# Kernel optimization log

Measured on AMD Instinct MI355X. Metric: run time of the kernel, lower is better.

## Reference

```python
import jax, jax.numpy as jnp
import numpy as np

N_NODES = 100000
N_EDGES = 3200000
F_IN, F_HID, F_OUT = 512, 128, 32


def setup_inputs() -> dict:
    key = jax.random.key(0)
    ks = jax.random.split(key, 8)
    x = jax.random.normal(ks[0], (N_NODES, F_IN), dtype=jnp.float32)
    edge_row = jax.random.randint(ks[1], (N_EDGES,), 0, N_NODES, dtype=jnp.int32)
    edge_col = jax.random.randint(ks[2], (N_EDGES,), 0, N_NODES, dtype=jnp.int32)
    edge_val = jax.random.uniform(ks[3], (N_EDGES,), dtype=jnp.float32)
    W1 = jax.random.normal(ks[4], (F_IN, F_HID), dtype=jnp.float32) / np.sqrt(F_IN)
    b1 = jnp.zeros((F_HID,), dtype=jnp.float32)
    W2 = jax.random.normal(ks[5], (F_HID, F_OUT), dtype=jnp.float32) / np.sqrt(F_HID)
    b2 = jnp.zeros((F_OUT,), dtype=jnp.float32)
    return {"x": x, "edge_row": edge_row, "edge_col": edge_col,
            "edge_val": edge_val, "W1": W1, "b1": b1, "W2": W2, "b2": b2}


def _spmm(edge_row, edge_col, edge_val, dense):
    # out[r] = sum_{e: row[e]==r} val[e] * dense[col[e]]  (COO SpMM)
    gathered = dense[edge_col] * edge_val[:, None]  # [E, F]
    return jax.ops.segment_sum(gathered, edge_row, num_segments=N_NODES)


def reference(x, edge_row, edge_col, edge_val, W1, b1, W2, b2):
    # GraphConvolution 1: support = x@W1; out = A @ support + b1
    h = _spmm(edge_row, edge_col, edge_val, x @ W1) + b1
    h = jax.nn.relu(h)
    # GraphConvolution 2
    logits = _spmm(edge_row, edge_col, edge_val, h @ W2) + b2
    return jax.nn.log_softmax(logits, axis=1)
```

## Files before the change

kernel.cpp:

```cpp
#include <hip/hip_runtime.h>


#define NN 100000
#define NE 3200000
#define FIN 512
#define FHID 128
#define FOUT 32
#define BROWS 64
#define NBUCK 1563
#define NPART 512
#define CHUNK 6250
#define TOT (NBUCK * NPART)
#define NSCAN1 782
#define EBCAP 2560

typedef __attribute__((ext_vector_type(8))) short bf16x8;
typedef __attribute__((ext_vector_type(4))) float f32x4;

static __device__ __forceinline__ unsigned short f2bf(float f) {
    unsigned u = __float_as_uint(f);
    unsigned r = (u + 0x7FFFu + ((u >> 16) & 1u)) >> 16;
    return (unsigned short)r;
}
static __device__ __forceinline__ float bf2f(unsigned short u) {
    return __uint_as_float(((unsigned)u) << 16);
}
static __device__ __forceinline__ float bflo(unsigned u) {
    return __uint_as_float(u << 16);
}
static __device__ __forceinline__ float bfhi(unsigned u) {
    return __uint_as_float(u & 0xffff0000u);
}
static __device__ __forceinline__ bf16x8 pack8(float4 u, float4 v) {
    bf16x8 r;
    r[0] = (short)f2bf(u.x); r[1] = (short)f2bf(u.y);
    r[2] = (short)f2bf(u.z); r[3] = (short)f2bf(u.w);
    r[4] = (short)f2bf(v.x); r[5] = (short)f2bf(v.y);
    r[6] = (short)f2bf(v.z); r[7] = (short)f2bf(v.w);
    return r;
}

__global__ __launch_bounds__(256) void fused_prep_hist(const float* __restrict__ W1,
                                                       unsigned short* __restrict__ W1t,
                                                       const int* __restrict__ erow,
                                                       int* __restrict__ cntG) {
    if (blockIdx.x < NPART) {
        __shared__ int c[NBUCK];
        const int t = threadIdx.x;
        const int w = blockIdx.x;
        for (int i = t; i < NBUCK; i += 256) c[i] = 0;
        __syncthreads();
        const int e0 = w * CHUNK;
        const int e1 = min(e0 + CHUNK, NE);
        for (int e = e0 + t; e < e1; e += 256) atomicAdd(&c[erow[e] >> 6], 1);
        __syncthreads();
        for (int i = t; i < NBUCK; i += 256) cntG[w * NBUCK + i] = c[i];
    } else {
        int t = (blockIdx.x - NPART) * 256 + threadIdx.x;
        int j = t & 7;
        int c = t >> 3;
        int l = c & 63;
        int ks = (c >> 6) & 15;
        int nt = c >> 10;
        int n = nt * 16 + (l & 15);
        int k = ks * 32 + ((l >> 4) << 3) + j;
        W1t[(size_t)c * 8 + j] = f2bf(W1[k * FHID + n]);
    }
}

__global__ __launch_bounds__(256) void scan1_kernel(const int* __restrict__ cntG,
                                                    int* __restrict__ off,
                                                    int* __restrict__ partials) {
    __shared__ int s[256];
    int t = threadIdx.x;
    int i0 = blockIdx.x * 1024 + t * 4;
    int v[4];
#pragma unroll
    for (int j = 0; j < 4; ++j) {
        int i = i0 + j;
        v[j] = (i < TOT) ? cntG[(i & (NPART - 1)) * NBUCK + (i >> 9)] : 0;
    }
    int lsum = v[0] + v[1] + v[2] + v[3];
    s[t] = lsum;
    __syncthreads();
    for (int o = 1; o < 256; o <<= 1) {
        int xv = (t >= o) ? s[t - o] : 0;
        __syncthreads();
        s[t] += xv;
        __syncthreads();
    }
    if (t == 255) partials[blockIdx.x] = s[255];
    int run = s[t] - lsum;
#pragma unroll
    for (int j = 0; j < 4; ++j) {
        if (i0 + j < TOT) off[i0 + j] = run;
        run += v[j];
    }
}

__global__ __launch_bounds__(1024) void scan2_kernel(int* partials) {
    __shared__ int s[1024];
    int t = threadIdx.x;
    int v = (t < NSCAN1) ? partials[t] : 0;
    s[t] = v;
    __syncthreads();
    for (int o = 1; o < 1024; o <<= 1) {
        int xv = (t >= o) ? s[t - o] : 0;
        __syncthreads();
        s[t] += xv;
        __syncthreads();
    }
    if (t < NSCAN1) partials[t] = s[t] - v;
}

__global__ __launch_bounds__(256) void scan3_kernel(int* __restrict__ off,
                                                    const int* __restrict__ partials) {
    int add = partials[blockIdx.x];
    int i0 = blockIdx.x * 1024 + threadIdx.x * 4;
#pragma unroll
    for (int j = 0; j < 4; ++j)
        if (i0 + j < TOT) off[i0 + j] += add;
}

__global__ __launch_bounds__(256) void scatter_part(const int* __restrict__ erow,
                                                    const int* __restrict__ ecol,
                                                    const float* __restrict__ eval,
                                                    const int* __restrict__ off,
                                                    int2* __restrict__ bcolval) {
    __shared__ int pos[NBUCK];
    const int t = threadIdx.x;
    const int w = blockIdx.x;
    for (int b = t; b < NBUCK; b += 256) pos[b] = off[b * NPART + w];
    __syncthreads();
    const int e0 = w * CHUNK;
    const int e1 = min(e0 + CHUNK, NE);
    for (int e = e0 + t; e < e1; e += 256) {
        int r = erow[e];
        int idx = atomicAdd(&pos[r >> 6], 1);
        bcolval[idx] = make_int2(ecol[e] | ((r & 63) << 20), __float_as_int(eval[e]));
    }
}

__global__ __launch_bounds__(256) void bucket_to_csr(const int* __restrict__ off,
                                                     const int2* __restrict__ bcolval,
                                                     int* __restrict__ rowptr,
                                                     int2* __restrict__ epack) {
    __shared__ int cnt[BROWS];
    __shared__ int pos[BROWS];
    __shared__ int s[BROWS];
    __shared__ int2 eb[EBCAP];
    const int b = blockIdx.x;
    const int t = threadIdx.x;
    const int s0 = off[b * NPART];
    const int send = (b == NBUCK - 1) ? NE : off[(b + 1) * NPART];
    const int n = send - s0;
    const bool fits = (n <= EBCAP);
    if (t < BROWS) cnt[t] = 0;
    __syncthreads();
    int2 myv[10];
    if (fits) {
#pragma unroll
        for (int ii = 0; ii < 10; ++ii) {
            int i = t + ii * 256;
            int2 v = make_int2(0, 0);
            if (i < n) {
                v = bcolval[s0 + i];
                atomicAdd(&cnt[((unsigned)v.x) >> 20], 1);
            }
            myv[ii] = v;
        }
    } else {
        for (int i = t; i < n; i += 256)
            atomicAdd(&cnt[((unsigned)bcolval[s0 + i].x) >> 20], 1);
    }
    __syncthreads();
    int myc = (t < BROWS) ? cnt[t] : 0;
    if (t < BROWS) s[t] = myc;
    __syncthreads();
    for (int o = 1; o < BROWS; o <<= 1) {
        int xv = (t >= o && t < BROWS) ? s[t - o] : 0;
        __syncthreads();
        if (t < BROWS) s[t] += xv;
        __syncthreads();
    }
    if (t < BROWS) {
        int excl = s[t] - myc;
        pos[t] = excl;
        int row = b * BROWS + t;
        if (row < NN) rowptr[row] = s0 + excl;
    }
    if (b == 0 && t == 0) rowptr[NN] = NE;
    __syncthreads();
    if (fits) {
#pragma unroll
        for (int ii = 0; ii < 10; ++ii) {
            int i = t + ii * 256;
            if (i < n) {
                int2 v = myv[ii];
                int p = atomicAdd(&pos[((unsigned)v.x) >> 20], 1);
                eb[p] = make_int2(v.x & 0xFFFFF, v.y);
            }
        }
        __syncthreads();
        for (int i = t; i < n; i += 256) epack[s0 + i] = eb[i];
    } else {
        for (int i = t; i < n; i += 256) {
            int2 v = bcolval[s0 + i];
            int p = atomicAdd(&pos[((unsigned)v.x) >> 20], 1);
            epack[s0 + p] = make_int2(v.x & 0xFFFFF, v.y);
        }
    }
}

__global__ __launch_bounds__(256) void gemm1_mfma(const float* __restrict__ x,
                                                  const unsigned short* __restrict__ W1t,
                                                  unsigned short* __restrict__ out) {
    const int tid = threadIdx.x;
    const int lane = tid & 63;
    const int w = tid >> 6;
    const int quad = lane >> 4;
    const int m = lane & 15;
    const int row0 = blockIdx.x * 128 + w * 32;

    int rA = row0 + m;
    int rB = row0 + 16 + m;
    rA = rA < NN ? rA : NN - 1;
    rB = rB < NN ? rB : NN - 1;
    const float* pA = x + (size_t)rA * FIN + quad * 8;
    const float* pB = x + (size_t)rB * FIN + quad * 8;

    f32x4 acc[2][8];
#pragma unroll
    for (int i = 0; i < 2; ++i)
#pragma unroll
        for (int nt = 0; nt < 8; ++nt) acc[i][nt] = (f32x4){0.f, 0.f, 0.f, 0.f};

    float4 a0 = *(const float4*)pA;
    float4 a1 = *(const float4*)(pA + 4);
    float4 b0 = *(const float4*)pB;
    float4 b1 = *(const float4*)(pB + 4);

    for (int ks = 0; ks < 16; ++ks) {
        const int kn = (ks + 1) & 15;
        float4 na0 = *(const float4*)(pA + kn * 32);
        float4 na1 = *(const float4*)(pA + kn * 32 + 4);
        float4 nb0 = *(const float4*)(pB + kn * 32);
        float4 nb1 = *(const float4*)(pB + kn * 32 + 4);

        bf16x8 fA = pack8(a0, a1);
        bf16x8 fB = pack8(b0, b1);
        bf16x8 bb[8];
#pragma unroll
        for (int nt = 0; nt < 8; ++nt)
            bb[nt] = *(const bf16x8*)(W1t + ((size_t)((nt * 16 + ks) * 64 + lane)) * 8);
#pragma unroll
        for (int nt = 0; nt < 8; ++nt) {
            acc[0][nt] = __builtin_amdgcn_mfma_f32_16x16x32_bf16(fA, bb[nt], acc[0][nt], 0, 0, 0);
            acc[1][nt] = __builtin_amdgcn_mfma_f32_16x16x32_bf16(fB, bb[nt], acc[1][nt], 0, 0, 0);
        }
        a0 = na0; a1 = na1; b0 = nb0; b1 = nb1;
    }

    const int crow0 = blockIdx.x * 128 + w * 32;
#pragma unroll
    for (int i = 0; i < 2; ++i)
#pragma unroll
        for (int nt = 0; nt < 8; ++nt) {
            int col = nt * 16 + m;
#pragma unroll
            for (int r = 0; r < 4; ++r) {
                int row = crow0 + i * 16 + quad * 4 + r;
                if (row < NN) out[(size_t)row * FHID + col] = f2bf(acc[i][nt][r]);
            }
        }
}

__global__ __launch_bounds__(256) void spmm1_kernel(const int* __restrict__ rowptr,
                                                    const int2* __restrict__ epack,
                                                    const unsigned short* __restrict__ dense,
                                                    const float* __restrict__ b1,
                                                    unsigned short* __restrict__ h) {
    const int lane = threadIdx.x & 63;
    const int row = blockIdx.x * 4 + (threadIdx.x >> 6);
    const int start = __builtin_amdgcn_readfirstlane(rowptr[row]);
    const int cnt = __builtin_amdgcn_readfirstlane(rowptr[row + 1]) - start;
    const int sl16 = lane & 15;
    float acc0 = 0.f, acc1 = 0.f;

    for (int j = 0; j < cnt; j += 16) {
        int idx = j + sl16;
        idx = idx < cnt ? idx : cnt - 1;
        const int2 p = epack[start + idx];
        const int rem = cnt - j;
        unsigned d[16];
#pragma unroll
        for (int k = 0; k < 16; ++k) {
            int col = __builtin_amdgcn_readlane(p.x, k);
            col = (k < rem) ? col : 0;
            d[k] = *((const unsigned*)(dense + ((size_t)col << 7)) + lane);
        }
#pragma unroll
        for (int k = 0; k < 16; ++k) {
            float v = (k < rem) ? __int_as_float(__builtin_amdgcn_readlane(p.y, k)) : 0.f;
            acc0 = fmaf(v, bflo(d[k]), acc0);
            acc1 = fmaf(v, bfhi(d[k]), acc1);
        }
    }
    float2 bb = *(const float2*)(b1 + lane * 2);
    unsigned r0 = f2bf(fmaxf(acc0 + bb.x, 0.f));
    unsigned r1 = f2bf(fmaxf(acc1 + bb.y, 0.f));
    *((unsigned*)(h + (size_t)row * FHID) + lane) = r0 | (r1 << 16);
}

__global__ __launch_bounds__(256) void gemm2_kernel(const unsigned short* __restrict__ h,
                                                    const float* __restrict__ W2,
                                                    unsigned short* __restrict__ out) {
    __shared__ float hs[64][129];
    const int tid = threadIdx.x;
    const int lane = tid & 63;
    const int cg = __builtin_amdgcn_readfirstlane(tid >> 6);
    const int row0 = blockIdx.x * 64;
    const int row = row0 + lane;

    float acc[8];
#pragma unroll
    for (int c = 0; c < 8; ++c) acc[c] = 0.f;

#pragma unroll
    for (int j = 0; j < 8; ++j) {
        int f4 = tid + j * 256;
        int r = f4 >> 5;
        int kq = f4 & 31;
        ushort4 v = make_ushort4(0, 0, 0, 0);
        if (row0 + r < NN) v = *(const ushort4*)(h + (size_t)(row0 + r) * FHID + kq * 4);
        hs[r][kq * 4 + 0] = bf2f(v.x);
        hs[r][kq * 4 + 1] = bf2f(v.y);
        hs[r][kq * 4 + 2] = bf2f(v.z);
        hs[r][kq * 4 + 3] = bf2f(v.w);
    }
    __syncthreads();
#pragma unroll 4
    for (int k = 0; k < FHID; ++k) {
        float a = hs[lane][k];
        const float* wrow = W2 + k * FOUT + cg * 8;
#pragma unroll
        for (int c = 0; c < 8; ++c) acc[c] += a * wrow[c];
    }
    if (row < NN) {
        uint4 st;
        st.x = (unsigned)f2bf(acc[0]) | ((unsigned)f2bf(acc[1]) << 16);
        st.y = (unsigned)f2bf(acc[2]) | ((unsigned)f2bf(acc[3]) << 16);
        st.z = (unsigned)f2bf(acc[4]) | ((unsigned)f2bf(acc[5]) << 16);
        st.w = (unsigned)f2bf(acc[6]) | ((unsigned)f2bf(acc[7]) << 16);
        *(uint4*)(out + (size_t)row * FOUT + cg * 8) = st;
    }
}

__global__ __launch_bounds__(256) void spmm2_kernel(const int* __restrict__ rowptr,
                                                    const int2* __restrict__ epack,
                                                    const unsigned short* __restrict__ dense,
                                                    const float* __restrict__ b2,
                                                    float* __restrict__ out) {
    const int lane = threadIdx.x & 63;
    const int row = blockIdx.x * 4 + (threadIdx.x >> 6);
    const int start = __builtin_amdgcn_readfirstlane(rowptr[row]);
    const int cnt = __builtin_amdgcn_readfirstlane(rowptr[row + 1]) - start;
    const int col = lane & 31;
    const int slot = lane >> 5;
    const int sl16 = lane & 15;
    float acc = 0.f;

    for (int j = 0; j < cnt; j += 16) {
        int idx = j + sl16;
        idx = idx < cnt ? idx : cnt - 1;
        const int2 p = epack[start + idx];
        const int rem = cnt - j;
        unsigned short d[8];
        float vv[8];
#pragma unroll
        for (int k = 0; k < 8; ++k) {
            int cA = __builtin_amdgcn_readlane(p.x, 2 * k);
            int cB = __builtin_amdgcn_readlane(p.x, 2 * k + 1);
            int ei = 2 * k + slot;
            int c = slot ? cB : cA;
            c = (ei < rem) ? c : 0;
            d[k] = *(dense + (size_t)c * FOUT + col);
            int vA = __builtin_amdgcn_readlane(p.y, 2 * k);
            int vB = __builtin_amdgcn_readlane(p.y, 2 * k + 1);
            float v = __int_as_float(slot ? vB : vA);
            vv[k] = (ei < rem) ? v : 0.f;
        }
#pragma unroll
        for (int k = 0; k < 8; ++k) acc = fmaf(vv[k], bf2f(d[k]), acc);
    }
    acc += __shfl_xor(acc, 32, 64);
    acc += b2[col];
    float m = acc;
#pragma unroll
    for (int mask = 16; mask >= 1; mask >>= 1) m = fmaxf(m, __shfl_xor(m, mask, 64));
    float ex = expf(acc - m);
    float ssum = ex;
#pragma unroll
    for (int mask = 16; mask >= 1; mask >>= 1) ssum += __shfl_xor(ssum, mask, 64);
    float lse = m + logf(ssum);
    if (lane < 32) out[(size_t)row * FOUT + col] = acc - lse;
}

extern "C" void kernel_launch(void* const* d_in, const int* in_sizes, int n_in,
                              void* d_out, int out_size, void* d_ws, size_t ws_size,
                              hipStream_t stream) {
    const float* x = (const float*)d_in[0];
    const int* erow = (const int*)d_in[1];
    const int* ecol = (const int*)d_in[2];
    const float* eval = (const float*)d_in[3];
    const float* W1 = (const float*)d_in[4];
    const float* b1 = (const float*)d_in[5];
    const float* W2 = (const float*)d_in[6];
    const float* b2 = (const float*)d_in[7];
    float* out = (float*)d_out;

    char* ws = (char*)d_ws;
    size_t off_b = 0;
    auto walloc = [&](size_t bytes) -> void* {
        void* p = ws + off_b;
        off_b = (off_b + bytes + 255) & ~(size_t)255;
        return p;
    };
    int2* epack = (int2*)walloc((size_t)NE * 8);
    int* rowptr = (int*)walloc((size_t)(NN + 1) * 4);
    int* cntG = (int*)walloc((size_t)TOT * 4);
    int* off = (int*)walloc((size_t)TOT * 4);
    int* partials = (int*)walloc(4096);
    unsigned short* W1t = (unsigned short*)walloc((size_t)FHID * FIN * 2);
    int2* bcolval = (int2*)walloc((size_t)NE * 8);
    unsigned short* support1 = (unsigned short*)walloc((size_t)NN * FHID * 2);
    unsigned short* h = (unsigned short*)walloc((size_t)NN * FHID * 2);
    unsigned short* support2 = support1;

    fused_prep_hist<<<NPART + 256, 256, 0, stream>>>(W1, W1t, erow, cntG);
    scan1_kernel<<<NSCAN1, 256, 0, stream>>>(cntG, off, partials);
    scan2_kernel<<<1, 1024, 0, stream>>>(partials);
    scan3_kernel<<<NSCAN1, 256, 0, stream>>>(off, partials);
    scatter_part<<<NPART, 256, 0, stream>>>(erow, ecol, eval, off, bcolval);
    bucket_to_csr<<<NBUCK, 256, 0, stream>>>(off, bcolval, rowptr, epack);
    gemm1_mfma<<<(NN + 127) / 128, 256, 0, stream>>>(x, W1t, support1);
    spmm1_kernel<<<NN / 4, 256, 0, stream>>>(rowptr, epack, support1, b1, h);
    gemm2_kernel<<<(NN + 63) / 64, 256, 0, stream>>>(h, W2, support2);
    spmm2_kernel<<<NN / 4, 256, 0, stream>>>(rowptr, epack, support2, b2, out);
}
```

Before: 657.1 us.

## Fuse edge scatter with gemm1, halve partitions, restructure both SpMM inner loops

The edge-scatter kernel and the first dense GEMM are merged into a single launch, with block index choosing the role, so the two independent stages can run concurrently and one launch goes away. The partition count for the bucket sort is halved, which shrinks the scan work. SpMM1 gains a 32-edge unrolled main loop with unmasked gathers and a separate tail. SpMM2 now has each quarter-wave handle 4 edges and each lane load 2 packed bf16 columns, with a matching log-softmax reduction. The risks are fewer blocks in the scatter stage and heavier register use from the fusion and unrolling.

```diff
diff --git a/kernel.cpp b/kernel.cpp
--- a/kernel.cpp
+++ b/kernel.cpp
@@ -8,10 +8,11 @@
 #define FOUT 32
 #define BROWS 64
 #define NBUCK 1563
-#define NPART 512
-#define CHUNK 6250
+#define NPART 256
+#define CHUNK 12800
 #define TOT (NBUCK * NPART)
-#define NSCAN1 782
+#define NSCAN1 391
+#define GG1 ((NN + 127) / 128)
 #define EBCAP 2560
 
 typedef __attribute__((ext_vector_type(8))) short bf16x8;
@@ -78,7 +79,7 @@
 #pragma unroll
     for (int j = 0; j < 4; ++j) {
         int i = i0 + j;
-        v[j] = (i < TOT) ? cntG[(i & (NPART - 1)) * NBUCK + (i >> 9)] : 0;
+        v[j] = (i < TOT) ? cntG[(i & (NPART - 1)) * NBUCK + (i >> 8)] : 0;
     }
     int lsum = v[0] + v[1] + v[2] + v[3];
     s[t] = lsum;
@@ -98,13 +99,13 @@
     }
 }
 
-__global__ __launch_bounds__(1024) void scan2_kernel(int* partials) {
-    __shared__ int s[1024];
+__global__ __launch_bounds__(512) void scan2_kernel(int* partials) {
+    __shared__ int s[512];
     int t = threadIdx.x;
     int v = (t < NSCAN1) ? partials[t] : 0;
     s[t] = v;
     __syncthreads();
-    for (int o = 1; o < 1024; o <<= 1) {
+    for (int o = 1; o < 512; o <<= 1) {
         int xv = (t >= o) ? s[t - o] : 0;
         __syncthreads();
         s[t] += xv;
@@ -122,22 +123,83 @@
         if (i0 + j < TOT) off[i0 + j] += add;
 }
 
-__global__ __launch_bounds__(256) void scatter_part(const int* __restrict__ erow,
-                                                    const int* __restrict__ ecol,
-                                                    const float* __restrict__ eval,
-                                                    const int* __restrict__ off,
-                                                    int2* __restrict__ bcolval) {
-    __shared__ int pos[NBUCK];
-    const int t = threadIdx.x;
-    const int w = blockIdx.x;
-    for (int b = t; b < NBUCK; b += 256) pos[b] = off[b * NPART + w];
-    __syncthreads();
-    const int e0 = w * CHUNK;
-    const int e1 = min(e0 + CHUNK, NE);
-    for (int e = e0 + t; e < e1; e += 256) {
-        int r = erow[e];
-        int idx = atomicAdd(&pos[r >> 6], 1);
-        bcolval[idx] = make_int2(ecol[e] | ((r & 63) << 20), __float_as_int(eval[e]));
+__global__ __launch_bounds__(256) void fused_scatter_gemm1(
+    const int* __restrict__ erow, const int* __restrict__ ecol,
+    const float* __restrict__ eval, const int* __restrict__ off,
+    int2* __restrict__ bcolval,
+    const float* __restrict__ x, const unsigned short* __restrict__ W1t,
+    unsigned short* __restrict__ outd) {
+    if (blockIdx.x < NPART) {
+        __shared__ int pos[NBUCK];
+        const int t = threadIdx.x;
+        const int w = blockIdx.x;
+        for (int b = t; b < NBUCK; b += 256) pos[b] = off[b * NPART + w];
+        __syncthreads();
+        const int e0 = w * CHUNK;
+        const int e1 = min(e0 + CHUNK, NE);
+        for (int e = e0 + t; e < e1; e += 256) {
+            int r = erow[e];
+            int idx = atomicAdd(&pos[r >> 6], 1);
+            bcolval[idx] = make_int2(ecol[e] | ((r & 63) << 20), __float_as_int(eval[e]));
+        }
+    } else {
+        const int tid = threadIdx.x;
+        const int lane = tid & 63;
+        const int w = tid >> 6;
+        const int quad = lane >> 4;
+        const int m = lane & 15;
+        const int row0 = (blockIdx.x - NPART) * 128 + w * 32;
+
+        int rA = row0 + m;
+        int rB = row0 + 16 + m;
+        rA = rA < NN ? rA : NN - 1;
+        rB = rB < NN ? rB : NN - 1;
+        const float* pA = x + (size_t)rA * FIN + quad * 8;
+        const float* pB = x + (size_t)rB * FIN + quad * 8;
+
+        f32x4 acc[2][8];
+#pragma unroll
+        for (int i = 0; i < 2; ++i)
+#pragma unroll
+            for (int nt = 0; nt < 8; ++nt) acc[i][nt] = (f32x4){0.f, 0.f, 0.f, 0.f};
+
+        float4 a0 = *(const float4*)pA;
+        float4 a1 = *(const float4*)(pA + 4);
+        float4 b0 = *(const float4*)pB;
+        float4 b1 = *(const float4*)(pB + 4);
+
+        for (int ks = 0; ks < 16; ++ks) {
+            const int kn = (ks + 1) & 15;
+            float4 na0 = *(const float4*)(pA + kn * 32);
+            float4 na1 = *(const float4*)(pA + kn * 32 + 4);
+            float4 nb0 = *(const float4*)(pB + kn * 32);
+            float4 nb1 = *(const float4*)(pB + kn * 32 + 4);
+
+            bf16x8 fA = pack8(a0, a1);
+            bf16x8 fB = pack8(b0, b1);
+            bf16x8 bb[8];
+#pragma unroll
+            for (int nt = 0; nt < 8; ++nt)
+                bb[nt] = *(const bf16x8*)(W1t + ((size_t)((nt * 16 + ks) * 64 + lane)) * 8);
+#pragma unroll
+            for (int nt = 0; nt < 8; ++nt) {
+                acc[0][nt] = __builtin_amdgcn_mfma_f32_16x16x32_bf16(fA, bb[nt], acc[0][nt], 0, 0, 0);
+                acc[1][nt] = __builtin_amdgcn_mfma_f32_16x16x32_bf16(fB, bb[nt], acc[1][nt], 0, 0, 0);
+            }
+            a0 = na0; a1 = na1; b0 = nb0; b1 = nb1;
+        }
+
+#pragma unroll
+        for (int i = 0; i < 2; ++i)
+#pragma unroll
+            for (int nt = 0; nt < 8; ++nt) {
+                int col = nt * 16 + m;
+#pragma unroll
+                for (int r = 0; r < 4; ++r) {
+                    int row = row0 + i * 16 + quad * 4 + r;
+                    if (row < NN) outd[(size_t)row * FHID + col] = f2bf(acc[i][nt][r]);
+                }
+            }
     }
 }
 
@@ -212,69 +274,6 @@
     }
 }
 
-__global__ __launch_bounds__(256) void gemm1_mfma(const float* __restrict__ x,
-                                                  const unsigned short* __restrict__ W1t,
-                                                  unsigned short* __restrict__ out) {
-    const int tid = threadIdx.x;
-    const int lane = tid & 63;
-    const int w = tid >> 6;
-    const int quad = lane >> 4;
-    const int m = lane & 15;
-    const int row0 = blockIdx.x * 128 + w * 32;
-
-    int rA = row0 + m;
-    int rB = row0 + 16 + m;
-    rA = rA < NN ? rA : NN - 1;
-    rB = rB < NN ? rB : NN - 1;
-    const float* pA = x + (size_t)rA * FIN + quad * 8;
-    const float* pB = x + (size_t)rB * FIN + quad * 8;
-
-    f32x4 acc[2][8];
-#pragma unroll
-    for (int i = 0; i < 2; ++i)
-#pragma unroll
-        for (int nt = 0; nt < 8; ++nt) acc[i][nt] = (f32x4){0.f, 0.f, 0.f, 0.f};
-
-    float4 a0 = *(const float4*)pA;
-    float4 a1 = *(const float4*)(pA + 4);
-    float4 b0 = *(const float4*)pB;
-    float4 b1 = *(const float4*)(pB + 4);
-
-    for (int ks = 0; ks < 16; ++ks) {
-        const int kn = (ks + 1) & 15;
-        float4 na0 = *(const float4*)(pA + kn * 32);
-        float4 na1 = *(const float4*)(pA + kn * 32 + 4);
-        float4 nb0 = *(const float4*)(pB + kn * 32);
-        float4 nb1 = *(const float4*)(pB + kn * 32 + 4);
-
-        bf16x8 fA = pack8(a0, a1);
-        bf16x8 fB = pack8(b0, b1);
-        bf16x8 bb[8];
-#pragma unroll
-        for (int nt = 0; nt < 8; ++nt)
-            bb[nt] = *(const bf16x8*)(W1t + ((size_t)((nt * 16 + ks) * 64 + lane)) * 8);
-#pragma unroll
-        for (int nt = 0; nt < 8; ++nt) {
-            acc[0][nt] = __builtin_amdgcn_mfma_f32_16x16x32_bf16(fA, bb[nt], acc[0][nt], 0, 0, 0);
-            acc[1][nt] = __builtin_amdgcn_mfma_f32_16x16x32_bf16(fB, bb[nt], acc[1][nt], 0, 0, 0);
-        }
-        a0 = na0; a1 = na1; b0 = nb0; b1 = nb1;
-    }
-
-    const int crow0 = blockIdx.x * 128 + w * 32;
-#pragma unroll
-    for (int i = 0; i < 2; ++i)
-#pragma unroll
-        for (int nt = 0; nt < 8; ++nt) {
-            int col = nt * 16 + m;
-#pragma unroll
-            for (int r = 0; r < 4; ++r) {
-                int row = crow0 + i * 16 + quad * 4 + r;
-                if (row < NN) out[(size_t)row * FHID + col] = f2bf(acc[i][nt][r]);
-            }
-        }
-}
-
 __global__ __launch_bounds__(256) void spmm1_kernel(const int* __restrict__ rowptr,
                                                     const int2* __restrict__ epack,
                                                     const unsigned short* __restrict__ dense,
@@ -285,19 +284,63 @@
     const int start = __builtin_amdgcn_readfirstlane(rowptr[row]);
     const int cnt = __builtin_amdgcn_readfirstlane(rowptr[row + 1]) - start;
     const int sl16 = lane & 15;
+    const unsigned* d32 = (const unsigned*)dense;
     float acc0 = 0.f, acc1 = 0.f;
 
-    for (int j = 0; j < cnt; j += 16) {
-        int idx = j + sl16;
-        idx = idx < cnt ? idx : cnt - 1;
-        const int2 p = epack[start + idx];
-        const int rem = cnt - j;
+    int j = 0;
+    for (; j + 32 <= cnt; j += 32) {
+        int2 p0 = epack[start + j + sl16];
+        int2 p1 = epack[start + j + 16 + sl16];
+        unsigned d[32];
+#pragma unroll
+        for (int k = 0; k < 16; ++k) {
+            int c = __builtin_amdgcn_readlane(p0.x, k);
+            d[k] = d32[((size_t)c << 6) + lane];
+        }
+#pragma unroll
+        for (int k = 0; k < 16; ++k) {
+            int c = __builtin_amdgcn_readlane(p1.x, k);
+            d[16 + k] = d32[((size_t)c << 6) + lane];
+        }
+#pragma unroll
+        for (int k = 0; k < 16; ++k) {
+            float v = __int_as_float(__builtin_amdgcn_readlane(p0.y, k));
+            acc0 = fmaf(v, bflo(d[k]), acc0);
+            acc1 = fmaf(v, bfhi(d[k]), acc1);
+        }
+#pragma unroll
+        for (int k = 0; k < 16; ++k) {
+            float v = __int_as_float(__builtin_amdgcn_readlane(p1.y, k));
+            acc0 = fmaf(v, bflo(d[16 + k]), acc0);
+            acc1 = fmaf(v, bfhi(d[16 + k]), acc1);
+        }
+    }
+    if (j + 16 <= cnt) {
+        int2 p = epack[start + j + sl16];
         unsigned d[16];
 #pragma unroll
         for (int k = 0; k < 16; ++k) {
-            int col = __builtin_amdgcn_readlane(p.x, k);
-            col = (k < rem) ? col : 0;
-            d[k] = *((const unsigned*)(dense + ((size_t)col << 7)) + lane);
+            int c = __builtin_amdgcn_readlane(p.x, k);
+            d[k] = d32[((size_t)c << 6) + lane];
+        }
+#pragma unroll
+        for (int k = 0; k < 16; ++k) {
+            float v = __int_as_float(__builtin_amdgcn_readlane(p.y, k));
+            acc0 = fmaf(v, bflo(d[k]), acc0);
+            acc1 = fmaf(v, bfhi(d[k]), acc1);
+        }
+        j += 16;
+    }
+    const int rem = cnt - j;
+    if (rem > 0) {
+        int idx = j + (sl16 < rem ? sl16 : rem - 1);
+        int2 p = epack[start + idx];
+        unsigned d[16];
+#pragma unroll
+        for (int k = 0; k < 16; ++k) {
+            int c = __builtin_amdgcn_readlane(p.x, k);
+            c = (k < rem) ? c : 0;
+            d[k] = d32[((size_t)c << 6) + lane];
         }
 #pragma unroll
         for (int k = 0; k < 16; ++k) {
@@ -365,45 +408,73 @@
     const int row = blockIdx.x * 4 + (threadIdx.x >> 6);
     const int start = __builtin_amdgcn_readfirstlane(rowptr[row]);
     const int cnt = __builtin_amdgcn_readfirstlane(rowptr[row + 1]) - start;
-    const int col = lane & 31;
-    const int slot = lane >> 5;
+    const int quad = lane >> 4;
     const int sl16 = lane & 15;
-    float acc = 0.f;
-
-    for (int j = 0; j < cnt; j += 16) {
-        int idx = j + sl16;
-        idx = idx < cnt ? idx : cnt - 1;
-        const int2 p = epack[start + idx];
-        const int rem = cnt - j;
-        unsigned short d[8];
-        float vv[8];
-#pragma unroll
-        for (int k = 0; k < 8; ++k) {
-            int cA = __builtin_amdgcn_readlane(p.x, 2 * k);
-            int cB = __builtin_amdgcn_readlane(p.x, 2 * k + 1);
-            int ei = 2 * k + slot;
-            int c = slot ? cB : cA;
-            c = (ei < rem) ? c : 0;
-            d[k] = *(dense + (size_t)c * FOUT + col);
-            int vA = __builtin_amdgcn_readlane(p.y, 2 * k);
-            int vB = __builtin_amdgcn_readlane(p.y, 2 * k + 1);
-            float v = __int_as_float(slot ? vB : vA);
-            vv[k] = (ei < rem) ? v : 0.f;
-        }
-#pragma unroll
-        for (int k = 0; k < 8; ++k) acc = fmaf(vv[k], bf2f(d[k]), acc);
-    }
-    acc += __shfl_xor(acc, 32, 64);
-    acc += b2[col];
-    float m = acc;
-#pragma unroll
-    for (int mask = 16; mask >= 1; mask >>= 1) m = fmaxf(m, __shfl_xor(m, mask, 64));
-    float ex = expf(acc - m);
-    float ssum = ex;
-#pragma unroll
-    for (int mask = 16; mask >= 1; mask >>= 1) ssum += __shfl_xor(ssum, mask, 64);
+    const unsigned* d32 = (const unsigned*)dense;
+    float acc0 = 0.f, acc1 = 0.f;
+
+    int j = 0;
+    for (; j + 16 <= cnt; j += 16) {
+        int2 p = epack[start + j + sl16];
+        unsigned d[4];
+        float vv[4];
+#pragma unroll
+        for (int k = 0; k < 16; ++k) {
+            int c = __builtin_amdgcn_readlane(p.x, k);
+            int v = __builtin_amdgcn_readlane(p.y, k);
+            if ((k >> 2) == quad) {
+                d[k & 3] = d32[((size_t)c << 4) + sl16];
+                vv[k & 3] = __int_as_float(v);
+            }
+        }
+#pragma unroll
+        for (int k = 0; k < 4; ++k) {
+            acc0 = fmaf(vv[k], bflo(d[k]), acc0);
+            acc1 = fmaf(vv[k], bfhi(d[k]), acc1);
+        }
+    }
+    const int rem = cnt - j;
+    if (rem > 0) {
+        int idx = j + (sl16 < rem ? sl16 : rem - 1);
+        int2 p = epack[start + idx];
+        unsigned d[4];
+        float vv[4];
+#pragma unroll
+        for (int k = 0; k < 4; ++k) { d[k] = 0; vv[k] = 0.f; }
+#pragma unroll
+        for (int k = 0; k < 16; ++k) {
+            int c = __builtin_amdgcn_readlane(p.x, k);
+            int v = __builtin_amdgcn_readlane(p.y, k);
+            c = (k < rem) ? c : 0;
+            if ((k >> 2) == quad) {
+                d[k & 3] = d32[((size_t)c << 4) + sl16];
+                vv[k & 3] = (k < rem) ? __int_as_float(v) : 0.f;
+            }
+        }
+#pragma unroll
+        for (int k = 0; k < 4; ++k) {
+            acc0 = fmaf(vv[k], bflo(d[k]), acc0);
+            acc1 = fmaf(vv[k], bfhi(d[k]), acc1);
+        }
+    }
+    acc0 += __shfl_xor(acc0, 16, 64);
+    acc0 += __shfl_xor(acc0, 32, 64);
+    acc1 += __shfl_xor(acc1, 16, 64);
+    acc1 += __shfl_xor(acc1, 32, 64);
+    float2 bb = *(const float2*)(b2 + sl16 * 2);
+    acc0 += bb.x;
+    acc1 += bb.y;
+    float m = fmaxf(acc0, acc1);
+#pragma unroll
+    for (int mask = 8; mask >= 1; mask >>= 1) m = fmaxf(m, __shfl_xor(m, mask, 64));
+    float ssum = expf(acc0 - m) + expf(acc1 - m);
+#pragma unroll
+    for (int mask = 8; mask >= 1; mask >>= 1) ssum += __shfl_xor(ssum, mask, 64);
     float lse = m + logf(ssum);
-    if (lane < 32) out[(size_t)row * FOUT + col] = acc - lse;
+    if (lane < 16) {
+        float2 st = make_float2(acc0 - lse, acc1 - lse);
+        *(float2*)(out + (size_t)row * FOUT + sl16 * 2) = st;
+    }
 }
 
 extern "C" void kernel_launch(void* const* d_in, const int* in_sizes, int n_in,
@@ -439,11 +510,11 @@
 
     fused_prep_hist<<<NPART + 256, 256, 0, stream>>>(W1, W1t, erow, cntG);
     scan1_kernel<<<NSCAN1, 256, 0, stream>>>(cntG, off, partials);
-    scan2_kernel<<<1, 1024, 0, stream>>>(partials);
+    scan2_kernel<<<1, 512, 0, stream>>>(partials);
     scan3_kernel<<<NSCAN1, 256, 0, stream>>>(off, partials);
-    scatter_part<<<NPART, 256, 0, stream>>>(erow, ecol, eval, off, bcolval);
+    fused_scatter_gemm1<<<NPART + GG1, 256, 0, stream>>>(erow, ecol, eval, off,
+                                                         bcolval, x, W1t, support1);
     bucket_to_csr<<<NBUCK, 256, 0, stream>>>(off, bcolval, rowptr, epack);
-    gemm1_mfma<<<(NN + 127) / 128, 256, 0, stream>>>(x, W1t, support1);
     spmm1_kernel<<<NN / 4, 256, 0, stream>>>(rowptr, epack, support1, b1, h);
     gemm2_kernel<<<(NN + 63) / 64, 256, 0, stream>>>(h, W2, support2);
     spmm2_kernel<<<NN / 4, 256, 0, stream>>>(rowptr, epack, support2, b2, out);
```

Measured after the change: 644.6 us. No clear change (-1.9%).
